# Optimization experiments

Hardware: AMD Instinct MI355X
Metric: run time of the kernel (lower is better)

Reference implementation:

```python
import jax, jax.numpy as jnp
import numpy as np

N = 6144
D_LAT = 512


def setup_inputs() -> dict:
    key = jax.random.key(0)
    k1, k2, k3 = jax.random.split(key, 3)
    latent = jax.random.normal(k1, (N, D_LAT), dtype=jnp.float32)
    coords = jax.random.normal(k2, (N, 3), dtype=jnp.float32)
    alpha = jax.random.uniform(k3, (N,), dtype=jnp.float32)
    return {"latent": latent, "coords": coords, "alpha": alpha}


def reference(latent, coords, alpha):
    # Pairwise Euclidean distances via the Gram trick (avoids [N,N,3] diff tensor).
    sq = jnp.sum(coords * coords, axis=-1)                      # [N]
    d2 = sq[:, None] + sq[None, :] - 2.0 * (coords @ coords.T)  # [N,N]
    # max with tiny eps keeps sqrt grad finite on the (zeroed-out) diagonal
    D = jnp.sqrt(jnp.maximum(d2, 1e-12)) + 1e-6                 # [N,N]
    a = 0.5 * (alpha[:, None] + alpha[None, :])                 # [N,N]
    K = jnp.clip(jnp.power(D, -a), 1e-8, 1000.0) * jnp.exp(-D / 12.0)
    K = K * (1.0 - jnp.eye(K.shape[0], dtype=K.dtype))          # zero diagonal
    K = K / (jnp.sum(K, axis=-1, keepdims=True) + 1e-8)         # row-normalize
    out = K @ latent                                            # [N,d]
    return out, K
```

## Files before the change

kernel.cpp:

```cpp
#include <hip/hip_runtime.h>
#include <hip/hip_bf16.h>

#define NN 6144
#define DLAT 512

typedef __attribute__((ext_vector_type(8))) short bf16x8;
typedef __attribute__((ext_vector_type(4))) float f32x4;

#define GLOAD_LDS16(g, l) \
  __builtin_amdgcn_global_load_lds((const __attribute__((address_space(1))) unsigned int*)(g), \
                                   (__attribute__((address_space(3))) unsigned int*)(l), 16, 0, 0)

__global__ __launch_bounds__(256) void prep_kernel(const float* __restrict__ coords,
                                                   const float* __restrict__ alpha,
                                                   float4* __restrict__ pre) {
  int j = blockIdx.x * 256 + threadIdx.x;
  if (j < NN) {
    pre[j] = make_float4(coords[3*j], coords[3*j+1], coords[3*j+2], alpha[j]);
  }
}

template<int USE_WS>
__global__ __launch_bounds__(256) void buildk_kernel(const float* __restrict__ coords,
                                                     const float* __restrict__ alpha,
                                                     const float4* __restrict__ pre,
                                                     float* __restrict__ Kout,
                                                     __hip_bfloat16* __restrict__ Kbf) {
  const int i = blockIdx.x;
  const int t = threadIdx.x;
  float ci0, ci1, ci2, ai;
  if constexpr (USE_WS) {
    float4 p = pre[i]; ci0 = p.x; ci1 = p.y; ci2 = p.z; ai = p.w;
  } else {
    ci0 = coords[3*i]; ci1 = coords[3*i+1]; ci2 = coords[3*i+2]; ai = alpha[i];
  }
  const float sqi = ci0*ci0 + ci1*ci1 + ci2*ci2;
  float vals[24];
  float lsum = 0.f;
#pragma unroll
  for (int it = 0; it < 24; ++it) {
    const int j = t + it*256;
    float c0, c1, c2, aj;
    if constexpr (USE_WS) {
      float4 p = pre[j]; c0 = p.x; c1 = p.y; c2 = p.z; aj = p.w;
    } else {
      c0 = coords[3*j]; c1 = coords[3*j+1]; c2 = coords[3*j+2]; aj = alpha[j];
    }
    float sqj = c0*c0 + c1*c1 + c2*c2;
    float dot = ci0*c0 + ci1*c1 + ci2*c2;
    float d2 = sqi + sqj - 2.f*dot;
    float D = sqrtf(fmaxf(d2, 1e-12f)) + 1e-6f;
    float a = 0.5f*(ai + aj);
    float p = __expf(-a * __logf(D));
    p = fminf(fmaxf(p, 1e-8f), 1000.f);
    float kv = p * __expf(D * (-1.f/12.f));
    if (j == i) kv = 0.f;
    vals[it] = kv;
    lsum += kv;
  }
#pragma unroll
  for (int off = 32; off > 0; off >>= 1) lsum += __shfl_down(lsum, off);
  __shared__ float red[4];
  if ((t & 63) == 0) red[t >> 6] = lsum;
  __syncthreads();
  const float inv = 1.f / (red[0] + red[1] + red[2] + red[3] + 1e-8f);
  const size_t rowoff = (size_t)i * NN;
#pragma unroll
  for (int it = 0; it < 24; ++it) {
    const int j = t + it*256;
    float v = vals[it] * inv;
    Kout[rowoff + j] = v;
    if constexpr (USE_WS) Kbf[rowoff + j] = __float2bfloat16(v);
  }
}

__global__ __launch_bounds__(256) void tlat_kernel(const float* __restrict__ latent,
                                                   __hip_bfloat16* __restrict__ lt) {
  __shared__ __hip_bfloat16 tile[64][65];
  const int t = threadIdx.x;
  const int kb = blockIdx.x * 64;
  const int nb = blockIdx.y * 64;
#pragma unroll
  for (int s = 0; s < 4; ++s) {
    int idx = t + s*256;
    int r = idx >> 4;
    int c4 = idx & 15;
    float4 v = *(const float4*)&latent[(size_t)(kb + r)*DLAT + nb + c4*4];
    tile[c4*4+0][r] = __float2bfloat16(v.x);
    tile[c4*4+1][r] = __float2bfloat16(v.y);
    tile[c4*4+2][r] = __float2bfloat16(v.z);
    tile[c4*4+3][r] = __float2bfloat16(v.w);
  }
  __syncthreads();
#pragma unroll
  for (int s = 0; s < 4; ++s) {
    int idx = t + s*256;
    int rr = idx >> 4;
    int cb = (idx & 15)*4;
#pragma unroll
    for (int q = 0; q < 4; ++q)
      lt[(size_t)(nb + rr)*NN + kb + cb + q] = tile[rr][cb + q];
  }
}

template<int SPLIT>
__global__ __launch_bounds__(256) void gemm_split_kernel(const __hip_bfloat16* __restrict__ A,
                                                         const __hip_bfloat16* __restrict__ B,
                                                         float* __restrict__ outp) {
  __shared__ __align__(16) short As[128*64];
  __shared__ __align__(16) short Bs[128*64];

  const int nwg = 48 * 4 * SPLIT;
  const int bx = blockIdx.x;
  const int wg = (bx % 8) * (nwg / 8) + bx / 8;
  const int row = wg / (4 * SPLIT);
  const int rem = wg % (4 * SPLIT);
  const int z   = rem / 4;
  const int col = rem % 4;
  const int rowBase = row * 128;
  const int colBase = col * 128;
  const int k0 = z * (NN / SPLIT);
  const int KSTEPS = (NN / SPLIT) / 64;

  const int t = threadIdx.x;
  const int lane = t & 63;
  const int w = t >> 6;
  const int wr = w >> 1;
  const int wc = w & 1;
  const int fr = lane & 15;
  const int fk = lane >> 4;

  const int srcg = (((lane & 7) ^ (lane >> 3)) << 4);
  const int lrow = lane >> 3;

  const char* Ab = (const char*)A;
  const char* Bb = (const char*)B;

  auto stage = [&](const char* src, short* dst, int rb, int kbyte) {
#pragma unroll
    for (int s = 0; s < 4; ++s) {
      const int c = w * 4 + s;
      const size_t goff = (size_t)(rb + c * 8 + lrow) * (NN * 2) + kbyte + srcg;
      GLOAD_LDS16(src + goff, dst + c * 512);
    }
  };

  auto rd = [&](const short* base, int r, int g) -> bf16x8 {
    return *(const bf16x8*)((const char*)base + r * 128 + (((g ^ (r & 7))) << 4));
  };

  f32x4 acc[4][4];
#pragma unroll
  for (int m = 0; m < 4; ++m)
#pragma unroll
    for (int n = 0; n < 4; ++n) acc[m][n] = (f32x4){0.f, 0.f, 0.f, 0.f};

  for (int kt = 0; kt < KSTEPS; ++kt) {
    const int kbyte = (k0 + kt * 64) * 2;
    stage(Ab, As, rowBase, kbyte);
    stage(Bb, Bs, colBase, kbyte);
    __syncthreads();
#pragma unroll
    for (int ks = 0; ks < 2; ++ks) {
      bf16x8 av[4], bv[4];
#pragma unroll
      for (int m = 0; m < 4; ++m) av[m] = rd(As, wr*64 + m*16 + fr, ks*4 + fk);
#pragma unroll
      for (int n = 0; n < 4; ++n) bv[n] = rd(Bs, wc*64 + n*16 + fr, ks*4 + fk);
#pragma unroll
      for (int m = 0; m < 4; ++m)
#pragma unroll
        for (int n = 0; n < 4; ++n)
          acc[m][n] = __builtin_amdgcn_mfma_f32_16x16x32_bf16(av[m], bv[n], acc[m][n], 0, 0, 0);
    }
    __syncthreads();
  }

  float* dst = outp + (SPLIT > 1 ? (size_t)z * NN * DLAT : 0);
#pragma unroll
  for (int m = 0; m < 4; ++m)
#pragma unroll
    for (int n = 0; n < 4; ++n) {
      const int row0 = rowBase + wr*64 + m*16 + fk*4;
      const int c0   = colBase + wc*64 + n*16 + fr;
#pragma unroll
      for (int i2 = 0; i2 < 4; ++i2)
        dst[(size_t)(row0 + i2) * DLAT + c0] = acc[m][n][i2];
    }
}

__global__ __launch_bounds__(256) void reduce_kernel(const float4* __restrict__ parts,
                                                     float4* __restrict__ out, int S) {
  const size_t stride = (size_t)NN * DLAT / 4;
  for (size_t idx = (size_t)blockIdx.x * 256 + threadIdx.x; idx < stride;
       idx += (size_t)gridDim.x * 256) {
    float4 a = parts[idx];
    for (int zz = 1; zz < S; ++zz) {
      float4 b = parts[idx + (size_t)zz * stride];
      a.x += b.x; a.y += b.y; a.z += b.z; a.w += b.w;
    }
    out[idx] = a;
  }
}

__global__ __launch_bounds__(256) void gemm_fallback(const float* __restrict__ Afp,
                                                     const float* __restrict__ Bfp,
                                                     float* __restrict__ out) {
  __shared__ __align__(16) short As[2][128][72];
  __shared__ __align__(16) short Bs[2][64][72];
  const int t = threadIdx.x;
  const int rowBase = blockIdx.x * 128;
  const int colBase = blockIdx.y * 64;
  const int lane = t & 63;
  const int w  = t >> 6;
  const int wr = w >> 1;
  const int wc = w & 1;
  const int fr = lane & 15;
  const int fk = lane >> 4;
  int4 ra[4], rb[2];

  auto load_regs = [&](int kt) {
#pragma unroll
    for (int s = 0; s < 4; ++s) {
      int c = t + s*256; int r = c >> 3, q = c & 7;
      const float* src = Afp + (size_t)(rowBase + r)*NN + kt*64 + q*8;
      float4 f0 = *(const float4*)src;
      float4 f1 = *(const float4*)(src + 4);
      __hip_bfloat16 h[8];
      h[0]=__float2bfloat16(f0.x); h[1]=__float2bfloat16(f0.y);
      h[2]=__float2bfloat16(f0.z); h[3]=__float2bfloat16(f0.w);
      h[4]=__float2bfloat16(f1.x); h[5]=__float2bfloat16(f1.y);
      h[6]=__float2bfloat16(f1.z); h[7]=__float2bfloat16(f1.w);
      ra[s] = *(const int4*)h;
    }
#pragma unroll
    for (int s = 0; s < 2; ++s) {
      int c = t + s*256; int r = c >> 3, q = c & 7;
      const float* src = Bfp + (size_t)(kt*64 + q*8)*DLAT + colBase + r;
      __hip_bfloat16 h[8];
#pragma unroll
      for (int i2 = 0; i2 < 8; ++i2) h[i2] = __float2bfloat16(src[(size_t)i2*DLAT]);
      rb[s] = *(const int4*)h;
    }
  };
  auto write_tiles = [&](int buf) {
#pragma unroll
    for (int s = 0; s < 4; ++s) {
      int c = t + s*256; int r = c >> 3, q = c & 7;
      *(int4*)&As[buf][r][q*8] = ra[s];
    }
#pragma unroll
    for (int s = 0; s < 2; ++s) {
      int c = t + s*256; int r = c >> 3, q = c & 7;
      *(int4*)&Bs[buf][r][q*8] = rb[s];
    }
  };
  f32x4 acc[4][2];
#pragma unroll
  for (int m = 0; m < 4; ++m)
#pragma unroll
    for (int n = 0; n < 2; ++n) acc[m][n] = (f32x4){0.f,0.f,0.f,0.f};
  auto compute = [&](int buf) {
#pragma unroll
    for (int ks = 0; ks < 2; ++ks) {
      bf16x8 av[4], bv[2];
#pragma unroll
      for (int m = 0; m < 4; ++m) av[m] = *(const bf16x8*)&As[buf][wr*64 + m*16 + fr][ks*32 + fk*8];
#pragma unroll
      for (int n = 0; n < 2; ++n) bv[n] = *(const bf16x8*)&Bs[buf][wc*32 + n*16 + fr][ks*32 + fk*8];
#pragma unroll
      for (int m = 0; m < 4; ++m)
#pragma unroll
        for (int n = 0; n < 2; ++n)
          acc[m][n] = __builtin_amdgcn_mfma_f32_16x16x32_bf16(av[m], bv[n], acc[m][n], 0, 0, 0);
    }
  };
  load_regs(0); write_tiles(0); __syncthreads();
  int buf = 0;
  for (int kt = 0; kt < 96; ++kt) {
    if (kt + 1 < 96) load_regs(kt + 1);
    compute(buf);
    if (kt + 1 < 96) write_tiles(buf ^ 1);
    __syncthreads();
    buf ^= 1;
  }
#pragma unroll
  for (int m = 0; m < 4; ++m)
#pragma unroll
    for (int n = 0; n < 2; ++n) {
      const int row0 = rowBase + wr*64 + m*16 + fk*4;
      const int c0   = colBase + wc*32 + n*16 + fr;
#pragma unroll
      for (int i2 = 0; i2 < 4; ++i2)
        out[(size_t)(row0 + i2)*DLAT + c0] = acc[m][n][i2];
    }
}

extern "C" void kernel_launch(void* const* d_in, const int* in_sizes, int n_in,
                              void* d_out, int out_size, void* d_ws, size_t ws_size,
                              hipStream_t stream) {
  const float* latent = (const float*)d_in[0];
  const float* coords = (const float*)d_in[1];
  const float* alpha  = (const float*)d_in[2];
  float* out  = (float*)d_out;
  float* Kout = out + (size_t)NN * DLAT;

  const size_t needK = (size_t)NN * NN * 2;
  const size_t needL = (size_t)DLAT * NN * 2;
  const size_t needP = (size_t)NN * 16;
  const size_t base  = needK + needL + needP;
  const size_t partB = (size_t)NN * DLAT * 4;

  if (ws_size >= base) {
    __hip_bfloat16* Kbf = (__hip_bfloat16*)d_ws;
    __hip_bfloat16* LT  = (__hip_bfloat16*)((char*)d_ws + needK);
    float4* pre = (float4*)((char*)d_ws + needK + needL);
    float* parts = (float*)((char*)d_ws + base);

    prep_kernel<<<NN/256, 256, 0, stream>>>(coords, alpha, pre);
    buildk_kernel<1><<<NN, 256, 0, stream>>>(coords, alpha, pre, Kout, Kbf);
    tlat_kernel<<<dim3(NN/64, DLAT/64), 256, 0, stream>>>(latent, LT);

    if (ws_size >= base + 4 * partB) {
      gemm_split_kernel<4><<<48*4*4, 256, 0, stream>>>(Kbf, LT, parts);
      reduce_kernel<<<768, 256, 0, stream>>>((const float4*)parts, (float4*)out, 4);
    } else if (ws_size >= base + 2 * partB) {
      gemm_split_kernel<2><<<48*4*2, 256, 0, stream>>>(Kbf, LT, parts);
      reduce_kernel<<<768, 256, 0, stream>>>((const float4*)parts, (float4*)out, 2);
    } else {
      gemm_split_kernel<1><<<48*4, 256, 0, stream>>>(Kbf, LT, out);
    }
  } else {
    buildk_kernel<0><<<NN, 256, 0, stream>>>(coords, alpha, nullptr, Kout, nullptr);
    gemm_fallback<<<dim3(NN/128, DLAT/64), 256, 0, stream>>>(Kout, latent, out);
  }
}
```

Before: 147.5 us.

## Fuse kernel-matrix generation into GEMM, precompute row sums separately

Replaces the separate build-K / bf16 K copy / transposed-latent / split GEMM pipeline with a first pass that computes only the row normalizers. A fused kernel then recomputes K tiles on the fly, writes the fp32 K output, and feeds bf16 tiles straight into MFMA with a 32-row by 512-column tile. This removes the bf16 K round trip through memory (about 75MB of writes and reads) and the latent transpose, in exchange for evaluating the transcendental kernel twice per element. The B operand is now repacked into 32-wide k blocks and read directly from global memory into registers without LDS staging.

```diff
diff --git a/kernel.cpp b/kernel.cpp
--- a/kernel.cpp
+++ b/kernel.cpp
@@ -20,32 +20,203 @@
   }
 }
 
-template<int USE_WS>
+__global__ __launch_bounds__(256) void rowinv_kernel(const float4* __restrict__ pre,
+                                                     float* __restrict__ inv) {
+  const int i0 = blockIdx.x * 8;
+  const int t = threadIdx.x;
+  const int lane = t & 63;
+  const int w = t >> 6;
+  float4 pi[8];
+  float sqi[8], ah[8], s[8];
+#pragma unroll
+  for (int r = 0; r < 8; ++r) {
+    pi[r] = pre[i0 + r];
+    sqi[r] = pi[r].x*pi[r].x + pi[r].y*pi[r].y + pi[r].z*pi[r].z;
+    ah[r] = 0.5f * pi[r].w;
+    s[r] = 0.f;
+  }
+  for (int j = t; j < NN; j += 256) {
+    float4 pj = pre[j];
+    float sqj = pj.x*pj.x + pj.y*pj.y + pj.z*pj.z;
+    float ajh = 0.5f * pj.w;
+#pragma unroll
+    for (int r = 0; r < 8; ++r) {
+      float dot = pi[r].x*pj.x + pi[r].y*pj.y + pi[r].z*pj.z;
+      float d2 = sqi[r] + sqj - 2.f*dot;
+      float D = sqrtf(fmaxf(d2, 1e-12f)) + 1e-6f;
+      float a = ah[r] + ajh;
+      float p = __expf(-a * __logf(D));
+      p = fminf(fmaxf(p, 1e-8f), 1000.f);
+      float v = p * __expf(D * (-1.f/12.f));
+      if (j == i0 + r) v = 0.f;
+      s[r] += v;
+    }
+  }
+#pragma unroll
+  for (int r = 0; r < 8; ++r)
+#pragma unroll
+    for (int off = 32; off > 0; off >>= 1) s[r] += __shfl_down(s[r], off);
+  __shared__ float red[8][4];
+  if (lane == 0) {
+#pragma unroll
+    for (int r = 0; r < 8; ++r) red[r][w] = s[r];
+  }
+  __syncthreads();
+  if (t < 8) inv[i0 + t] = 1.f / (red[t][0] + red[t][1] + red[t][2] + red[t][3] + 1e-8f);
+}
+
+__global__ __launch_bounds__(256) void btile_kernel(const float* __restrict__ latent,
+                                                    __hip_bfloat16* __restrict__ BT) {
+  const int jt = blockIdx.x;
+  const int col = blockIdx.y * 256 + threadIdx.x;
+  float v[32];
+#pragma unroll
+  for (int q = 0; q < 32; ++q)
+    v[q] = latent[(size_t)(jt*32 + q)*DLAT + col];
+  __hip_bfloat16* dst = BT + ((size_t)jt * DLAT + col) * 32;
+#pragma unroll
+  for (int g = 0; g < 4; ++g) {
+    __hip_bfloat16 hb[8];
+#pragma unroll
+    for (int q = 0; q < 8; ++q) hb[q] = __float2bfloat16(v[g*8 + q]);
+    *(bf16x8*)(dst + g*8) = *(const bf16x8*)hb;
+  }
+}
+
+template<int SPLIT>
+__global__ __launch_bounds__(256) void fused_kernel(const float4* __restrict__ pre,
+                                                    const float* __restrict__ inv,
+                                                    const __hip_bfloat16* __restrict__ BT,
+                                                    float* __restrict__ Kout,
+                                                    float* __restrict__ parts) {
+  __shared__ __align__(16) short As[32 * 64];
+  __shared__ __align__(16) float4 preJ[64];
+
+  const int nwg = (NN/32) * SPLIT;
+  const int bx = blockIdx.x;
+  const int wg = (bx & 7) * (nwg >> 3) + (bx >> 3);
+  const int rowblk = wg % (NN/32);
+  const int z = wg / (NN/32);
+  const int rowBase = rowblk * 32;
+  const int k0 = z * (NN / SPLIT);
+  const int KSTEPS = (NN / SPLIT) / 64;
+
+  const int t = threadIdx.x;
+  const int lane = t & 63;
+  const int w = t >> 6;
+  const int fr = lane & 15;
+  const int fk = lane >> 4;
+  const int colW = w * 128;
+
+  const int r  = t >> 3;
+  const int jg = t & 7;
+  const int irow = rowBase + r;
+  const float4 pi = pre[irow];
+  const float sqi = pi.x*pi.x + pi.y*pi.y + pi.z*pi.z;
+  const float ahalf = 0.5f * pi.w;
+  const float rinv = inv[irow];
+
+  auto rdA = [&](int rr, int g) -> bf16x8 {
+    return *(const bf16x8*)((const char*)As + rr*128 + ((g ^ (rr & 7)) << 4));
+  };
+
+  f32x4 acc[2][8];
+#pragma unroll
+  for (int m = 0; m < 2; ++m)
+#pragma unroll
+    for (int n = 0; n < 8; ++n) acc[m][n] = (f32x4){0.f, 0.f, 0.f, 0.f};
+
+  for (int kt = 0; kt < KSTEPS; ++kt) {
+    const int j0 = k0 + kt * 64;
+    if (w == 0) GLOAD_LDS16(pre + j0 + lane, preJ);
+    bf16x8 bvp[2][8];
+#pragma unroll
+    for (int ks = 0; ks < 2; ++ks) {
+      const size_t btbase = (size_t)((j0 >> 5) + ks) * (DLAT * 32);
+#pragma unroll
+      for (int n = 0; n < 8; ++n)
+        bvp[ks][n] = *(const bf16x8*)(BT + btbase + (size_t)(colW + n*16 + fr)*32 + fk*8);
+    }
+    __syncthreads();
+
+    float kv[8];
+#pragma unroll
+    for (int q = 0; q < 8; ++q) {
+      float4 pj = preJ[jg*8 + q];
+      float sqj = pj.x*pj.x + pj.y*pj.y + pj.z*pj.z;
+      float dot = pi.x*pj.x + pi.y*pj.y + pi.z*pj.z;
+      float d2 = sqi + sqj - 2.f*dot;
+      float D = sqrtf(fmaxf(d2, 1e-12f)) + 1e-6f;
+      float a = ahalf + 0.5f*pj.w;
+      float p = __expf(-a * __logf(D));
+      p = fminf(fmaxf(p, 1e-8f), 1000.f);
+      float v = p * __expf(D * (-1.f/12.f));
+      if (j0 + jg*8 + q == irow) v = 0.f;
+      kv[q] = v * rinv;
+    }
+    {
+      float* kdst = Kout + (size_t)irow * NN + j0 + jg*8;
+      *(float4*)kdst = make_float4(kv[0], kv[1], kv[2], kv[3]);
+      *(float4*)(kdst + 4) = make_float4(kv[4], kv[5], kv[6], kv[7]);
+      __hip_bfloat16 hb[8];
+#pragma unroll
+      for (int q = 0; q < 8; ++q) hb[q] = __float2bfloat16(kv[q]);
+      *(bf16x8*)((char*)As + r*128 + ((jg ^ (r & 7)) << 4)) = *(const bf16x8*)hb;
+    }
+    __syncthreads();
+
+#pragma unroll
+    for (int ks = 0; ks < 2; ++ks) {
+      bf16x8 av0 = rdA(fr,      ks*4 + fk);
+      bf16x8 av1 = rdA(16 + fr, ks*4 + fk);
+#pragma unroll
+      for (int n = 0; n < 8; ++n) {
+        acc[0][n] = __builtin_amdgcn_mfma_f32_16x16x32_bf16(av0, bvp[ks][n], acc[0][n], 0, 0, 0);
+        acc[1][n] = __builtin_amdgcn_mfma_f32_16x16x32_bf16(av1, bvp[ks][n], acc[1][n], 0, 0, 0);
+      }
+    }
+  }
+
+  float* dst = parts + (size_t)z * NN * DLAT;
+#pragma unroll
+  for (int m = 0; m < 2; ++m)
+#pragma unroll
+    for (int n = 0; n < 8; ++n) {
+      const int row0 = rowBase + m*16 + fk*4;
+      const int c0   = colW + n*16 + fr;
+#pragma unroll
+      for (int i2 = 0; i2 < 4; ++i2)
+        dst[(size_t)(row0 + i2)*DLAT + c0] = acc[m][n][i2];
+    }
+}
+
+__global__ __launch_bounds__(256) void reduce_kernel(const float4* __restrict__ parts,
+                                                     float4* __restrict__ out, int S) {
+  const size_t stride = (size_t)NN * DLAT / 4;
+  for (size_t idx = (size_t)blockIdx.x * 256 + threadIdx.x; idx < stride;
+       idx += (size_t)gridDim.x * 256) {
+    float4 a = parts[idx];
+    for (int zz = 1; zz < S; ++zz) {
+      float4 b = parts[idx + (size_t)zz * stride];
+      a.x += b.x; a.y += b.y; a.z += b.z; a.w += b.w;
+    }
+    out[idx] = a;
+  }
+}
+
 __global__ __launch_bounds__(256) void buildk_kernel(const float* __restrict__ coords,
                                                      const float* __restrict__ alpha,
-                                                     const float4* __restrict__ pre,
-                                                     float* __restrict__ Kout,
-                                                     __hip_bfloat16* __restrict__ Kbf) {
+                                                     float* __restrict__ Kout) {
   const int i = blockIdx.x;
   const int t = threadIdx.x;
-  float ci0, ci1, ci2, ai;
-  if constexpr (USE_WS) {
-    float4 p = pre[i]; ci0 = p.x; ci1 = p.y; ci2 = p.z; ai = p.w;
-  } else {
-    ci0 = coords[3*i]; ci1 = coords[3*i+1]; ci2 = coords[3*i+2]; ai = alpha[i];
-  }
+  float ci0 = coords[3*i], ci1 = coords[3*i+1], ci2 = coords[3*i+2], ai = alpha[i];
   const float sqi = ci0*ci0 + ci1*ci1 + ci2*ci2;
   float vals[24];
   float lsum = 0.f;
 #pragma unroll
   for (int it = 0; it < 24; ++it) {
     const int j = t + it*256;
-    float c0, c1, c2, aj;
-    if constexpr (USE_WS) {
-      float4 p = pre[j]; c0 = p.x; c1 = p.y; c2 = p.z; aj = p.w;
-    } else {
-      c0 = coords[3*j]; c1 = coords[3*j+1]; c2 = coords[3*j+2]; aj = alpha[j];
-    }
+    float c0 = coords[3*j], c1 = coords[3*j+1], c2 = coords[3*j+2], aj = alpha[j];
     float sqj = c0*c0 + c1*c1 + c2*c2;
     float dot = ci0*c0 + ci1*c1 + ci2*c2;
     float d2 = sqi + sqj - 2.f*dot;
@@ -66,141 +237,7 @@
   const float inv = 1.f / (red[0] + red[1] + red[2] + red[3] + 1e-8f);
   const size_t rowoff = (size_t)i * NN;
 #pragma unroll
-  for (int it = 0; it < 24; ++it) {
-    const int j = t + it*256;
-    float v = vals[it] * inv;
-    Kout[rowoff + j] = v;
-    if constexpr (USE_WS) Kbf[rowoff + j] = __float2bfloat16(v);
-  }
-}
-
-__global__ __launch_bounds__(256) void tlat_kernel(const float* __restrict__ latent,
-                                                   __hip_bfloat16* __restrict__ lt) {
-  __shared__ __hip_bfloat16 tile[64][65];
-  const int t = threadIdx.x;
-  const int kb = blockIdx.x * 64;
-  const int nb = blockIdx.y * 64;
-#pragma unroll
-  for (int s = 0; s < 4; ++s) {
-    int idx = t + s*256;
-    int r = idx >> 4;
-    int c4 = idx & 15;
-    float4 v = *(const float4*)&latent[(size_t)(kb + r)*DLAT + nb + c4*4];
-    tile[c4*4+0][r] = __float2bfloat16(v.x);
-    tile[c4*4+1][r] = __float2bfloat16(v.y);
-    tile[c4*4+2][r] = __float2bfloat16(v.z);
-    tile[c4*4+3][r] = __float2bfloat16(v.w);
-  }
-  __syncthreads();
-#pragma unroll
-  for (int s = 0; s < 4; ++s) {
-    int idx = t + s*256;
-    int rr = idx >> 4;
-    int cb = (idx & 15)*4;
-#pragma unroll
-    for (int q = 0; q < 4; ++q)
-      lt[(size_t)(nb + rr)*NN + kb + cb + q] = tile[rr][cb + q];
-  }
-}
-
-template<int SPLIT>
-__global__ __launch_bounds__(256) void gemm_split_kernel(const __hip_bfloat16* __restrict__ A,
-                                                         const __hip_bfloat16* __restrict__ B,
-                                                         float* __restrict__ outp) {
-  __shared__ __align__(16) short As[128*64];
-  __shared__ __align__(16) short Bs[128*64];
-
-  const int nwg = 48 * 4 * SPLIT;
-  const int bx = blockIdx.x;
-  const int wg = (bx % 8) * (nwg / 8) + bx / 8;
-  const int row = wg / (4 * SPLIT);
-  const int rem = wg % (4 * SPLIT);
-  const int z   = rem / 4;
-  const int col = rem % 4;
-  const int rowBase = row * 128;
-  const int colBase = col * 128;
-  const int k0 = z * (NN / SPLIT);
-  const int KSTEPS = (NN / SPLIT) / 64;
-
-  const int t = threadIdx.x;
-  const int lane = t & 63;
-  const int w = t >> 6;
-  const int wr = w >> 1;
-  const int wc = w & 1;
-  const int fr = lane & 15;
-  const int fk = lane >> 4;
-
-  const int srcg = (((lane & 7) ^ (lane >> 3)) << 4);
-  const int lrow = lane >> 3;
-
-  const char* Ab = (const char*)A;
-  const char* Bb = (const char*)B;
-
-  auto stage = [&](const char* src, short* dst, int rb, int kbyte) {
-#pragma unroll
-    for (int s = 0; s < 4; ++s) {
-      const int c = w * 4 + s;
-      const size_t goff = (size_t)(rb + c * 8 + lrow) * (NN * 2) + kbyte + srcg;
-      GLOAD_LDS16(src + goff, dst + c * 512);
-    }
-  };
-
-  auto rd = [&](const short* base, int r, int g) -> bf16x8 {
-    return *(const bf16x8*)((const char*)base + r * 128 + (((g ^ (r & 7))) << 4));
-  };
-
-  f32x4 acc[4][4];
-#pragma unroll
-  for (int m = 0; m < 4; ++m)
-#pragma unroll
-    for (int n = 0; n < 4; ++n) acc[m][n] = (f32x4){0.f, 0.f, 0.f, 0.f};
-
-  for (int kt = 0; kt < KSTEPS; ++kt) {
-    const int kbyte = (k0 + kt * 64) * 2;
-    stage(Ab, As, rowBase, kbyte);
-    stage(Bb, Bs, colBase, kbyte);
-    __syncthreads();
-#pragma unroll
-    for (int ks = 0; ks < 2; ++ks) {
-      bf16x8 av[4], bv[4];
-#pragma unroll
-      for (int m = 0; m < 4; ++m) av[m] = rd(As, wr*64 + m*16 + fr, ks*4 + fk);
-#pragma unroll
-      for (int n = 0; n < 4; ++n) bv[n] = rd(Bs, wc*64 + n*16 + fr, ks*4 + fk);
-#pragma unroll
-      for (int m = 0; m < 4; ++m)
-#pragma unroll
-        for (int n = 0; n < 4; ++n)
-          acc[m][n] = __builtin_amdgcn_mfma_f32_16x16x32_bf16(av[m], bv[n], acc[m][n], 0, 0, 0);
-    }
-    __syncthreads();
-  }
-
-  float* dst = outp + (SPLIT > 1 ? (size_t)z * NN * DLAT : 0);
-#pragma unroll
-  for (int m = 0; m < 4; ++m)
-#pragma unroll
-    for (int n = 0; n < 4; ++n) {
-      const int row0 = rowBase + wr*64 + m*16 + fk*4;
-      const int c0   = colBase + wc*64 + n*16 + fr;
-#pragma unroll
-      for (int i2 = 0; i2 < 4; ++i2)
-        dst[(size_t)(row0 + i2) * DLAT + c0] = acc[m][n][i2];
-    }
-}
-
-__global__ __launch_bounds__(256) void reduce_kernel(const float4* __restrict__ parts,
-                                                     float4* __restrict__ out, int S) {
-  const size_t stride = (size_t)NN * DLAT / 4;
-  for (size_t idx = (size_t)blockIdx.x * 256 + threadIdx.x; idx < stride;
-       idx += (size_t)gridDim.x * 256) {
-    float4 a = parts[idx];
-    for (int zz = 1; zz < S; ++zz) {
-      float4 b = parts[idx + (size_t)zz * stride];
-      a.x += b.x; a.y += b.y; a.z += b.z; a.w += b.w;
-    }
-    out[idx] = a;
-  }
+  for (int it = 0; it < 24; ++it) Kout[rowoff + t + it*256] = vals[it] * inv;
 }
 
 __global__ __launch_bounds__(256) void gemm_fallback(const float* __restrict__ Afp,
@@ -218,7 +255,6 @@
   const int fr = lane & 15;
   const int fk = lane >> 4;
   int4 ra[4], rb[2];
-
   auto load_regs = [&](int kt) {
 #pragma unroll
     for (int s = 0; s < 4; ++s) {
@@ -305,33 +341,24 @@
   float* out  = (float*)d_out;
   float* Kout = out + (size_t)NN * DLAT;
 
-  const size_t needK = (size_t)NN * NN * 2;
-  const size_t needL = (size_t)DLAT * NN * 2;
+  const size_t needB = (size_t)NN * DLAT * 2;
   const size_t needP = (size_t)NN * 16;
-  const size_t base  = needK + needL + needP;
-  const size_t partB = (size_t)NN * DLAT * 4;
-
-  if (ws_size >= base) {
-    __hip_bfloat16* Kbf = (__hip_bfloat16*)d_ws;
-    __hip_bfloat16* LT  = (__hip_bfloat16*)((char*)d_ws + needK);
-    float4* pre = (float4*)((char*)d_ws + needK + needL);
-    float* parts = (float*)((char*)d_ws + base);
+  const size_t needI = (size_t)NN * 4;
+  const size_t needS = 2 * (size_t)NN * DLAT * 4;
+
+  if (ws_size >= needB + needP + needI + needS) {
+    __hip_bfloat16* BT = (__hip_bfloat16*)d_ws;
+    float4* pre  = (float4*)((char*)d_ws + needB);
+    float* inv   = (float*)((char*)d_ws + needB + needP);
+    float* parts = (float*)((char*)d_ws + needB + needP + needI);
 
     prep_kernel<<<NN/256, 256, 0, stream>>>(coords, alpha, pre);
-    buildk_kernel<1><<<NN, 256, 0, stream>>>(coords, alpha, pre, Kout, Kbf);
-    tlat_kernel<<<dim3(NN/64, DLAT/64), 256, 0, stream>>>(latent, LT);
-
-    if (ws_size >= base + 4 * partB) {
-      gemm_split_kernel<4><<<48*4*4, 256, 0, stream>>>(Kbf, LT, parts);
-      reduce_kernel<<<768, 256, 0, stream>>>((const float4*)parts, (float4*)out, 4);
-    } else if (ws_size >= base + 2 * partB) {
-      gemm_split_kernel<2><<<48*4*2, 256, 0, stream>>>(Kbf, LT, parts);
-      reduce_kernel<<<768, 256, 0, stream>>>((const float4*)parts, (float4*)out, 2);
-    } else {
-      gemm_split_kernel<1><<<48*4, 256, 0, stream>>>(Kbf, LT, out);
-    }
+    btile_kernel<<<dim3(NN/32, DLAT/256), 256, 0, stream>>>(latent, BT);
+    rowinv_kernel<<<NN/8, 256, 0, stream>>>(pre, inv);
+    fused_kernel<2><<<(NN/32)*2, 256, 0, stream>>>(pre, inv, BT, Kout, parts);
+    reduce_kernel<<<768, 256, 0, stream>>>((const float4*)parts, (float4*)out, 2);
   } else {
-    buildk_kernel<0><<<NN, 256, 0, stream>>>(coords, alpha, nullptr, Kout, nullptr);
+    buildk_kernel<<<NN, 256, 0, stream>>>(coords, alpha, Kout);
     gemm_fallback<<<dim3(NN/128, DLAT/64), 256, 0, stream>>>(Kout, latent, out);
   }
 }
```

Measured after the change: 197.8 us. +34.2%, slower.
